# Performance work log

Measured on AMD Instinct MI355X. Metric: run time of the kernel, lower is better.

The kernel has to match this reference:

```python
import jax, jax.numpy as jnp
import numpy as np

T = 0.2
EPS = 1e-05


def setup_inputs() -> dict:
    key = jax.random.key(0)
    k1, k2 = jax.random.split(key)
    N, D, NUM_CLASSES = 8192, 128, 128
    inp = jax.random.normal(k1, (N, D), dtype=jnp.float32)
    label = jax.random.randint(k2, (N,), 0, NUM_CLASSES, dtype=jnp.int64)
    return {"input": inp, "label": label}


def reference(input, label):
    # Pairwise cosine similarity: dot(x_i, x_j) / max(||x_i|| * ||x_j||, eps)
    norms = jnp.sqrt(jnp.sum(input * input, axis=1))            # [N]
    denom = jnp.maximum(norms[:, None] * norms[None, :], EPS)   # [N, N]
    sim = (input @ input.T) / denom                             # [N, N]

    mask = (label[:, None] == label[None, :]).astype(input.dtype)  # same-label mask
    e = jnp.exp(sim / T)
    e = e - jnp.diag(jnp.diag(e))                               # zero the diagonal

    pos = mask * e                                              # positives (diag already 0)
    unsim = jnp.sum(e - pos, axis=-1, keepdims=True)            # [N, 1] negatives row-sum
    ratio = pos / (pos + unsim)                                 # per-pair NT-Xent prob
    safe = jnp.where(ratio > 0, ratio, 1.0)                     # loss[loss<=0] = 1
    loss_sum = jnp.sum(-jnp.log(safe))

    # number of off-diagonal positive pairs
    off_diag_mask = mask - jnp.diag(jnp.diag(mask))
    n_pos = jnp.count_nonzero(off_diag_mask).astype(input.dtype)
    return loss_sum / n_pos
```

## Files before the change

### kernel.cpp

```cpp
#include <hip/hip_runtime.h>
#include <math.h>

typedef float f32x4 __attribute__((ext_vector_type(4)));
typedef __attribute__((address_space(3))) unsigned int lds_u32;
typedef __attribute__((address_space(1))) const unsigned int glb_u32;

__global__ __launch_bounds__(256) void norm_kernel(
    const float* __restrict__ X, unsigned char* __restrict__ Y8,
    float* __restrict__ out, float inv_sqrtT) {
  int t = threadIdx.x;
  int row = blockIdx.x * 8 + (t >> 5);
  int l32 = t & 31;
  float4 v = ((const float4*)(X + (size_t)row * 128))[l32];
  float s = v.x * v.x + v.y * v.y + v.z * v.z + v.w * v.w;
  s += __shfl_xor(s, 1);
  s += __shfl_xor(s, 2);
  s += __shfl_xor(s, 4);
  s += __shfl_xor(s, 8);
  s += __shfl_xor(s, 16);
  float inv = inv_sqrtT * rsqrtf(fmaxf(s, 1e-24f));
  int pk = __builtin_amdgcn_cvt_pk_fp8_f32(v.x * inv, v.y * inv, 0, false);
  pk = __builtin_amdgcn_cvt_pk_fp8_f32(v.z * inv, v.w * inv, pk, true);
  int chunk = l32 >> 2;
  int off = ((chunk ^ (row & 7)) << 4) + ((l32 & 3) << 2);
  *(unsigned int*)(Y8 + (size_t)row * 128 + off) = (unsigned)pk;
  if (blockIdx.x == 0 && t == 0) out[0] = 0.f;
}

__global__ __launch_bounds__(256, 4) void pass1_kernel(
    const unsigned char* __restrict__ Y8, const int* __restrict__ lab,
    float* __restrict__ P, float* __restrict__ Q, float* __restrict__ S,
    int N) {
  __shared__ unsigned char As[128][128];
  __shared__ unsigned char Bs[2][64][128];
  __shared__ int labR[128];
  __shared__ float sS[4];

  const int b = blockIdx.x;
  const int bi = b >> 4, c = b & 15;
  const int i0 = bi * 128;
  const int j0 = c * 512;
  const int t = threadIdx.x;
  const int w = t >> 6, lane = t & 63;

#pragma unroll
  for (int k = 0; k < 4; ++k) {
    const int c0 = w * 64 + k * 256;
    const int cc = c0 + lane;
    __builtin_amdgcn_global_load_lds(
        (glb_u32*)(Y8 + (size_t)i0 * 128 + (size_t)cc * 16),
        (lds_u32*)((unsigned char*)&As[0][0] + c0 * 16), 16, 0, 0);
  }
#pragma unroll
  for (int k = 0; k < 2; ++k) {
    const int c0 = w * 64 + k * 256;
    const int cc = c0 + lane;
    __builtin_amdgcn_global_load_lds(
        (glb_u32*)(Y8 + (size_t)j0 * 128 + (size_t)cc * 16),
        (lds_u32*)((unsigned char*)&Bs[0][0][0] + c0 * 16), 16, 0, 0);
  }
  if (t < 128) labR[t] = lab[i0 + t];
  __syncthreads();

  const int quad = lane >> 4, l16 = lane & 15;
  const int rbase = w * 32;
  const int sw = l16 & 7;

  int lr[2][4];
#pragma unroll
  for (int pi = 0; pi < 2; ++pi)
#pragma unroll
    for (int r = 0; r < 4; ++r)
      lr[pi][r] = labR[rbase + pi * 16 + quad * 4 + r];

  float trow[2][4] = {};
  float pr[2][4] = {};
  float sacc = 0.f;

  for (int jt = 0; jt < 8; ++jt) {
    const int cur = jt & 1;
    const int jt0 = j0 + jt * 64;

    if (jt < 7) {
      const unsigned char* src = Y8 + (size_t)(jt0 + 64) * 128;
      unsigned char* dst = (unsigned char*)&Bs[cur ^ 1][0][0];
#pragma unroll
      for (int k = 0; k < 2; ++k) {
        const int c0 = w * 64 + k * 256;
        const int cc = c0 + lane;
        __builtin_amdgcn_global_load_lds((glb_u32*)(src + (size_t)cc * 16),
                                         (lds_u32*)(dst + c0 * 16), 16, 0, 0);
      }
    }

    int lc[4], cg[4];
#pragma unroll
    for (int pj = 0; pj < 4; ++pj) {
      cg[pj] = jt0 + pj * 16 + l16;
      lc[pj] = lab[cg[pj]];
    }

    f32x4 acc[2][4] = {};
#pragma unroll
    for (int ks = 0; ks < 4; ++ks) {
      const int ch = ks * 2 + (quad >> 1);
      const int off = ((ch ^ sw) << 4) + ((quad & 1) << 3);
      long af[2], bf[4];
#pragma unroll
      for (int p = 0; p < 2; ++p)
        af[p] = *(const long*)&As[rbase + p * 16 + l16][off];
#pragma unroll
      for (int p = 0; p < 4; ++p)
        bf[p] = *(const long*)&Bs[cur][p * 16 + l16][off];
#pragma unroll
      for (int pi = 0; pi < 2; ++pi)
#pragma unroll
        for (int pj = 0; pj < 4; ++pj)
          acc[pi][pj] = __builtin_amdgcn_mfma_f32_16x16x32_fp8_fp8(
              af[pi], bf[pj], acc[pi][pj], 0, 0, 0);
    }

    const bool dphase = ((jt0 >> 7) == bi);
    if (dphase) {
#pragma unroll
      for (int pi = 0; pi < 2; ++pi)
#pragma unroll
        for (int pj = 0; pj < 4; ++pj)
#pragma unroll
          for (int r = 0; r < 4; ++r) {
            const float s = acc[pi][pj][r];
            const float e = __expf(s);
            const int rowl = rbase + pi * 16 + quad * 4 + r;
            const bool self = (i0 + rowl) == cg[pj];
            const bool match = (lr[pi][r] == lc[pj]) && !self;
            trow[pi][r] += self ? 0.f : e;
            pr[pi][r] += match ? e : 0.f;
            sacc += match ? s : 0.f;
          }
    } else {
#pragma unroll
      for (int pi = 0; pi < 2; ++pi)
#pragma unroll
        for (int pj = 0; pj < 4; ++pj)
#pragma unroll
          for (int r = 0; r < 4; ++r) {
            const float s = acc[pi][pj][r];
            const float e = __expf(s);
            const bool match = (lr[pi][r] == lc[pj]);
            trow[pi][r] += e;
            pr[pi][r] += match ? e : 0.f;
            sacc += match ? s : 0.f;
          }
    }
    __syncthreads();
  }

#pragma unroll
  for (int pi = 0; pi < 2; ++pi)
#pragma unroll
    for (int r = 0; r < 4; ++r) {
      float v = trow[pi][r], q = pr[pi][r];
      v += __shfl_xor(v, 1);
      q += __shfl_xor(q, 1);
      v += __shfl_xor(v, 2);
      q += __shfl_xor(q, 2);
      v += __shfl_xor(v, 4);
      q += __shfl_xor(q, 4);
      v += __shfl_xor(v, 8);
      q += __shfl_xor(q, 8);
      if (l16 == 0) {
        const int row = rbase + pi * 16 + quad * 4 + r;
        P[c * N + i0 + row] = v;
        Q[c * N + i0 + row] = q;
      }
    }
#pragma unroll
  for (int m = 1; m < 64; m <<= 1) sacc += __shfl_xor(sacc, m);
  if (lane == 0) sS[w] = sacc;
  __syncthreads();
  if (t == 0) S[b] = sS[0] + sS[1] + sS[2] + sS[3];
}

__global__ __launch_bounds__(256) void finalize_kernel(
    const int* __restrict__ lab, const float* __restrict__ P,
    const float* __restrict__ Q, const float* __restrict__ S,
    float* __restrict__ out, int N) {
  __shared__ int hist[256];
  __shared__ float red[4];
  const int b = blockIdx.x, t = threadIdx.x;
  const int lane = t & 63, w = t >> 6;
  hist[t] = 0;
  __syncthreads();
  for (int i = t; i < N; i += 256) atomicAdd(&hist[lab[i] & 255], 1);
  __syncthreads();

  const int i = b * 256 + t;
  float tot = 0.f, p = 0.f;
#pragma unroll
  for (int cc = 0; cc < 16; ++cc) {
    tot += P[cc * N + i];
    p += Q[cc * N + i];
  }
  const float u = tot - p;
  const float cnti = (float)(hist[lab[i] & 255] - 1);
  float local = cnti * __logf(u) + p / u;
  if (t < 32) local -= S[b * 32 + t];
#pragma unroll
  for (int m = 1; m < 64; m <<= 1) local += __shfl_xor(local, m);
  if (lane == 0) red[w] = local;
  __syncthreads();
  if (t == 0) {
    float np = 0.f;
    for (int k = 0; k < 256; ++k) {
      const float m = (float)hist[k];
      np += m * m;
    }
    atomicAdd(out, (red[0] + red[1] + red[2] + red[3]) / (np - (float)N));
  }
}

extern "C" void kernel_launch(void* const* d_in, const int* in_sizes, int n_in,
                              void* d_out, int out_size, void* d_ws,
                              size_t ws_size, hipStream_t stream) {
  const float* X = (const float*)d_in[0];
  const int* lab = (const int*)d_in[1];
  float* out = (float*)d_out;

  const int N = in_sizes[1];

  unsigned char* Y8 = (unsigned char*)d_ws;
  float* P = (float*)(Y8 + (size_t)N * 128);
  float* Q = P + 16 * (size_t)N;
  float* S = Q + 16 * (size_t)N;

  const float inv_sqrtT = 2.2360679775f;
  norm_kernel<<<N / 8, 256, 0, stream>>>(X, Y8, out, inv_sqrtT);

  const int nblk = (N / 128) * 16;
  pass1_kernel<<<nblk, 256, 0, stream>>>(Y8, lab, P, Q, S, N);
  finalize_kernel<<<N / 256, 256, 0, stream>>>(lab, P, Q, S, out, N);
}
```

Before: 98.40 us.

## Drop LDS staging, load fp8 MFMA fragments from global, use exp2 scaling

Removes the LDS tiles and the async global-to-LDS double buffering. The A fragments are now kept in registers and the B fragments are read straight from global memory (the tile is small and should hit in cache), which also drops the per-tile barriers and the swizzled layout. The input scale now folds in log2(e), so the kernel can use exp2f in place of expf, and the diagonal-sum term is converted back by multiplying with ln2. The cost is more global and L2 traffic per MFMA with no LDS reuse across waves, and loads may be less coalesced.

New measurement: 138.7 us. 1.41x slower.

```diff
diff --git a/kernel.cpp b/kernel.cpp
--- a/kernel.cpp
+++ b/kernel.cpp
@@ -2,12 +2,11 @@
 #include <math.h>
 
 typedef float f32x4 __attribute__((ext_vector_type(4)));
-typedef __attribute__((address_space(3))) unsigned int lds_u32;
-typedef __attribute__((address_space(1))) const unsigned int glb_u32;
+
 
 __global__ __launch_bounds__(256) void norm_kernel(
     const float* __restrict__ X, unsigned char* __restrict__ Y8,
-    float* __restrict__ out, float inv_sqrtT) {
+    float* __restrict__ out, float scaleAB) {
   int t = threadIdx.x;
   int row = blockIdx.x * 8 + (t >> 5);
   int l32 = t & 31;
@@ -18,12 +17,10 @@
   s += __shfl_xor(s, 4);
   s += __shfl_xor(s, 8);
   s += __shfl_xor(s, 16);
-  float inv = inv_sqrtT * rsqrtf(fmaxf(s, 1e-24f));
+  float inv = scaleAB * rsqrtf(fmaxf(s, 1e-24f));
   int pk = __builtin_amdgcn_cvt_pk_fp8_f32(v.x * inv, v.y * inv, 0, false);
   pk = __builtin_amdgcn_cvt_pk_fp8_f32(v.z * inv, v.w * inv, pk, true);
-  int chunk = l32 >> 2;
-  int off = ((chunk ^ (row & 7)) << 4) + ((l32 & 3) << 2);
-  *(unsigned int*)(Y8 + (size_t)row * 128 + off) = (unsigned)pk;
+  *(unsigned int*)(Y8 + (size_t)row * 128 + l32 * 4) = (unsigned)pk;
   if (blockIdx.x == 0 && t == 0) out[0] = 0.f;
 }
 
@@ -31,9 +28,6 @@
     const unsigned char* __restrict__ Y8, const int* __restrict__ lab,
     float* __restrict__ P, float* __restrict__ Q, float* __restrict__ S,
     int N) {
-  __shared__ unsigned char As[128][128];
-  __shared__ unsigned char Bs[2][64][128];
-  __shared__ int labR[128];
   __shared__ float sS[4];
 
   const int b = blockIdx.x;
@@ -42,82 +36,53 @@
   const int j0 = c * 512;
   const int t = threadIdx.x;
   const int w = t >> 6, lane = t & 63;
-
-#pragma unroll
-  for (int k = 0; k < 4; ++k) {
-    const int c0 = w * 64 + k * 256;
-    const int cc = c0 + lane;
-    __builtin_amdgcn_global_load_lds(
-        (glb_u32*)(Y8 + (size_t)i0 * 128 + (size_t)cc * 16),
-        (lds_u32*)((unsigned char*)&As[0][0] + c0 * 16), 16, 0, 0);
-  }
-#pragma unroll
-  for (int k = 0; k < 2; ++k) {
-    const int c0 = w * 64 + k * 256;
-    const int cc = c0 + lane;
-    __builtin_amdgcn_global_load_lds(
-        (glb_u32*)(Y8 + (size_t)j0 * 128 + (size_t)cc * 16),
-        (lds_u32*)((unsigned char*)&Bs[0][0][0] + c0 * 16), 16, 0, 0);
-  }
-  if (t < 128) labR[t] = lab[i0 + t];
-  __syncthreads();
-
   const int quad = lane >> 4, l16 = lane & 15;
   const int rbase = w * 32;
-  const int sw = l16 & 7;
+  const int colb = quad * 8;
+
+  long af[4][2];
+#pragma unroll
+  for (int ks = 0; ks < 4; ++ks)
+#pragma unroll
+    for (int p = 0; p < 2; ++p)
+      af[ks][p] = *(const long*)(Y8 +
+                                 (size_t)(i0 + rbase + p * 16 + l16) * 128 +
+                                 ks * 32 + colb);
 
   int lr[2][4];
 #pragma unroll
   for (int pi = 0; pi < 2; ++pi)
 #pragma unroll
     for (int r = 0; r < 4; ++r)
-      lr[pi][r] = labR[rbase + pi * 16 + quad * 4 + r];
+      lr[pi][r] = lab[i0 + rbase + pi * 16 + quad * 4 + r];
 
   float trow[2][4] = {};
   float pr[2][4] = {};
   float sacc = 0.f;
 
+#pragma unroll 2
   for (int jt = 0; jt < 8; ++jt) {
-    const int cur = jt & 1;
     const int jt0 = j0 + jt * 64;
 
-    if (jt < 7) {
-      const unsigned char* src = Y8 + (size_t)(jt0 + 64) * 128;
-      unsigned char* dst = (unsigned char*)&Bs[cur ^ 1][0][0];
-#pragma unroll
-      for (int k = 0; k < 2; ++k) {
-        const int c0 = w * 64 + k * 256;
-        const int cc = c0 + lane;
-        __builtin_amdgcn_global_load_lds((glb_u32*)(src + (size_t)cc * 16),
-                                         (lds_u32*)(dst + c0 * 16), 16, 0, 0);
-      }
-    }
-
-    int lc[4], cg[4];
-#pragma unroll
-    for (int pj = 0; pj < 4; ++pj) {
-      cg[pj] = jt0 + pj * 16 + l16;
-      lc[pj] = lab[cg[pj]];
-    }
+    int lc[4];
+#pragma unroll
+    for (int pj = 0; pj < 4; ++pj) lc[pj] = lab[jt0 + pj * 16 + l16];
 
     f32x4 acc[2][4] = {};
 #pragma unroll
     for (int ks = 0; ks < 4; ++ks) {
-      const int ch = ks * 2 + (quad >> 1);
-      const int off = ((ch ^ sw) << 4) + ((quad & 1) << 3);
-      long af[2], bf[4];
-#pragma unroll
-      for (int p = 0; p < 2; ++p)
-        af[p] = *(const long*)&As[rbase + p * 16 + l16][off];
+      long bf[4];
 #pragma unroll
       for (int p = 0; p < 4; ++p)
-        bf[p] = *(const long*)&Bs[cur][p * 16 + l16][off];
+        bf[p] = *(const long*)(Y8 +
+                               (size_t)(jt0 + p * 16 + l16) * 128 +
+                               ks * 32 + colb);
 #pragma unroll
       for (int pi = 0; pi < 2; ++pi)
 #pragma unroll
         for (int pj = 0; pj < 4; ++pj)
           acc[pi][pj] = __builtin_amdgcn_mfma_f32_16x16x32_fp8_fp8(
-              af[pi], bf[pj], acc[pi][pj], 0, 0, 0);
+              af[ks][pi], bf[pj], acc[pi][pj], 0, 0, 0);
     }
 
     const bool dphase = ((jt0 >> 7) == bi);
@@ -128,14 +93,14 @@
         for (int pj = 0; pj < 4; ++pj)
 #pragma unroll
           for (int r = 0; r < 4; ++r) {
-            const float s = acc[pi][pj][r];
-            const float e = __expf(s);
+            const float s2 = acc[pi][pj][r];
+            const float e = exp2f(s2);
             const int rowl = rbase + pi * 16 + quad * 4 + r;
-            const bool self = (i0 + rowl) == cg[pj];
+            const bool self = (i0 + rowl) == (jt0 + pj * 16 + l16);
             const bool match = (lr[pi][r] == lc[pj]) && !self;
             trow[pi][r] += self ? 0.f : e;
             pr[pi][r] += match ? e : 0.f;
-            sacc += match ? s : 0.f;
+            sacc += match ? s2 : 0.f;
           }
     } else {
 #pragma unroll
@@ -144,15 +109,14 @@
         for (int pj = 0; pj < 4; ++pj)
 #pragma unroll
           for (int r = 0; r < 4; ++r) {
-            const float s = acc[pi][pj][r];
-            const float e = __expf(s);
+            const float s2 = acc[pi][pj][r];
+            const float e = exp2f(s2);
             const bool match = (lr[pi][r] == lc[pj]);
             trow[pi][r] += e;
             pr[pi][r] += match ? e : 0.f;
-            sacc += match ? s : 0.f;
+            sacc += match ? s2 : 0.f;
           }
     }
-    __syncthreads();
   }
 
 #pragma unroll
@@ -178,7 +142,8 @@
   for (int m = 1; m < 64; m <<= 1) sacc += __shfl_xor(sacc, m);
   if (lane == 0) sS[w] = sacc;
   __syncthreads();
-  if (t == 0) S[b] = sS[0] + sS[1] + sS[2] + sS[3];
+  if (t == 0)
+    S[b] = (sS[0] + sS[1] + sS[2] + sS[3]) * 0.69314718056f;
 }
 
 __global__ __launch_bounds__(256) void finalize_kernel(
@@ -233,10 +198,11 @@
   float* Q = P + 16 * (size_t)N;
   float* S = Q + 16 * (size_t)N;
 
-  const float inv_sqrtT = 2.2360679775f;
-  norm_kernel<<<N / 8, 256, 0, stream>>>(X, Y8, out, inv_sqrtT);
+  const float scaleAB = 2.68579102f;
+
+  norm_kernel<<<N / 8, 256, 0, stream>>>(X, Y8, out, scaleAB);
 
   const int nblk = (N / 128) * 16;
   pass1_kernel<<<nblk, 256, 0, stream>>>(Y8, lab, P, Q, S, N);
-  finalize_kernel<<<N / 256, 256, 0, stream>>>(lab, P, Q, S, out, N);
-}
+  finalize_kernel<<<32, 256, 0, stream>>>(lab, P, Q, S, out, N);
+}
```

## Shrink row tile to 64, keep A fragments in registers, fold exp scale into base 2

Applied to the files above, without the earlier changes.

Each block of the similarity pass now covers 64 rows instead of 128. A fragments are loaded straight from global memory into registers, so the As LDS tile and label staging are gone, and launch bounds allow 6 waves per SIMD. The normalisation scale now includes the factor log2(e), so the kernel can use exp2f. The positive-similarity sum is multiplied by ln2 to compensate. The grid doubles and B tiles are reloaded twice as often per row, trading less reuse for higher occupancy and cheaper exponentials.

Measured after the change: 100.4 us. About the same (+2.0%).

```diff
diff --git a/kernel.cpp b/kernel.cpp
--- a/kernel.cpp
+++ b/kernel.cpp
@@ -5,9 +5,10 @@
 typedef __attribute__((address_space(3))) unsigned int lds_u32;
 typedef __attribute__((address_space(1))) const unsigned int glb_u32;
 
+
 __global__ __launch_bounds__(256) void norm_kernel(
     const float* __restrict__ X, unsigned char* __restrict__ Y8,
-    float* __restrict__ out, float inv_sqrtT) {
+    float* __restrict__ out, float scaleAB) {
   int t = threadIdx.x;
   int row = blockIdx.x * 8 + (t >> 5);
   int l32 = t & 31;
@@ -18,7 +19,7 @@
   s += __shfl_xor(s, 4);
   s += __shfl_xor(s, 8);
   s += __shfl_xor(s, 16);
-  float inv = inv_sqrtT * rsqrtf(fmaxf(s, 1e-24f));
+  float inv = scaleAB * rsqrtf(fmaxf(s, 1e-24f));
   int pk = __builtin_amdgcn_cvt_pk_fp8_f32(v.x * inv, v.y * inv, 0, false);
   pk = __builtin_amdgcn_cvt_pk_fp8_f32(v.z * inv, v.w * inv, pk, true);
   int chunk = l32 >> 2;
@@ -27,30 +28,23 @@
   if (blockIdx.x == 0 && t == 0) out[0] = 0.f;
 }
 
-__global__ __launch_bounds__(256, 4) void pass1_kernel(
+__global__ __launch_bounds__(256, 6) void pass1_kernel(
     const unsigned char* __restrict__ Y8, const int* __restrict__ lab,
     float* __restrict__ P, float* __restrict__ Q, float* __restrict__ S,
     int N) {
-  __shared__ unsigned char As[128][128];
   __shared__ unsigned char Bs[2][64][128];
-  __shared__ int labR[128];
   __shared__ float sS[4];
 
   const int b = blockIdx.x;
   const int bi = b >> 4, c = b & 15;
-  const int i0 = bi * 128;
+  const int i0 = bi * 64;
   const int j0 = c * 512;
   const int t = threadIdx.x;
   const int w = t >> 6, lane = t & 63;
-
-#pragma unroll
-  for (int k = 0; k < 4; ++k) {
-    const int c0 = w * 64 + k * 256;
-    const int cc = c0 + lane;
-    __builtin_amdgcn_global_load_lds(
-        (glb_u32*)(Y8 + (size_t)i0 * 128 + (size_t)cc * 16),
-        (lds_u32*)((unsigned char*)&As[0][0] + c0 * 16), 16, 0, 0);
-  }
+  const int quad = lane >> 4, l16 = lane & 15;
+  const int rbase = w * 16;
+  const int sw = l16 & 7;
+
 #pragma unroll
   for (int k = 0; k < 2; ++k) {
     const int c0 = w * 64 + k * 256;
@@ -59,23 +53,26 @@
         (glb_u32*)(Y8 + (size_t)j0 * 128 + (size_t)cc * 16),
         (lds_u32*)((unsigned char*)&Bs[0][0][0] + c0 * 16), 16, 0, 0);
   }
-  if (t < 128) labR[t] = lab[i0 + t];
-  __syncthreads();
-
-  const int quad = lane >> 4, l16 = lane & 15;
-  const int rbase = w * 32;
-  const int sw = l16 & 7;
-
-  int lr[2][4];
-#pragma unroll
-  for (int pi = 0; pi < 2; ++pi)
-#pragma unroll
-    for (int r = 0; r < 4; ++r)
-      lr[pi][r] = labR[rbase + pi * 16 + quad * 4 + r];
-
-  float trow[2][4] = {};
-  float pr[2][4] = {};
+
+  long af[4];
+  {
+    const size_t abase = (size_t)(i0 + rbase + l16) * 128;
+#pragma unroll
+    for (int ks = 0; ks < 4; ++ks) {
+      const int ch = ks * 2 + (quad >> 1);
+      const int off = ((ch ^ sw) << 4) + ((quad & 1) << 3);
+      af[ks] = *(const long*)(Y8 + abase + off);
+    }
+  }
+  int lr[4];
+#pragma unroll
+  for (int r = 0; r < 4; ++r) lr[r] = lab[i0 + rbase + quad * 4 + r];
+
+  float trow[4] = {};
+  float pr[4] = {};
   float sacc = 0.f;
+
+  __syncthreads();
 
   for (int jt = 0; jt < 8; ++jt) {
     const int cur = jt & 1;
@@ -93,92 +90,78 @@
       }
     }
 
-    int lc[4], cg[4];
-#pragma unroll
-    for (int pj = 0; pj < 4; ++pj) {
-      cg[pj] = jt0 + pj * 16 + l16;
-      lc[pj] = lab[cg[pj]];
-    }
-
-    f32x4 acc[2][4] = {};
+    int lc[4];
+#pragma unroll
+    for (int pj = 0; pj < 4; ++pj) lc[pj] = lab[jt0 + pj * 16 + l16];
+
+    f32x4 acc[4] = {};
 #pragma unroll
     for (int ks = 0; ks < 4; ++ks) {
       const int ch = ks * 2 + (quad >> 1);
       const int off = ((ch ^ sw) << 4) + ((quad & 1) << 3);
-      long af[2], bf[4];
-#pragma unroll
-      for (int p = 0; p < 2; ++p)
-        af[p] = *(const long*)&As[rbase + p * 16 + l16][off];
+      long bf[4];
 #pragma unroll
       for (int p = 0; p < 4; ++p)
         bf[p] = *(const long*)&Bs[cur][p * 16 + l16][off];
 #pragma unroll
-      for (int pi = 0; pi < 2; ++pi)
-#pragma unroll
-        for (int pj = 0; pj < 4; ++pj)
-          acc[pi][pj] = __builtin_amdgcn_mfma_f32_16x16x32_fp8_fp8(
-              af[pi], bf[pj], acc[pi][pj], 0, 0, 0);
-    }
-
-    const bool dphase = ((jt0 >> 7) == bi);
-    if (dphase) {
-#pragma unroll
-      for (int pi = 0; pi < 2; ++pi)
-#pragma unroll
-        for (int pj = 0; pj < 4; ++pj)
-#pragma unroll
-          for (int r = 0; r < 4; ++r) {
-            const float s = acc[pi][pj][r];
-            const float e = __expf(s);
-            const int rowl = rbase + pi * 16 + quad * 4 + r;
-            const bool self = (i0 + rowl) == cg[pj];
-            const bool match = (lr[pi][r] == lc[pj]) && !self;
-            trow[pi][r] += self ? 0.f : e;
-            pr[pi][r] += match ? e : 0.f;
-            sacc += match ? s : 0.f;
-          }
+      for (int pj = 0; pj < 4; ++pj)
+        acc[pj] = __builtin_amdgcn_mfma_f32_16x16x32_fp8_fp8(af[ks], bf[pj],
+                                                             acc[pj], 0, 0, 0);
+    }
+
+    if (jt0 == i0) {
+#pragma unroll
+      for (int pj = 0; pj < 4; ++pj)
+#pragma unroll
+        for (int r = 0; r < 4; ++r) {
+          const float s2 = acc[pj][r];
+          const float e = exp2f(s2);
+          const int rowl = rbase + quad * 4 + r;
+          const bool self = rowl == (pj * 16 + l16);
+          const bool match = (lr[r] == lc[pj]) && !self;
+          trow[r] += self ? 0.f : e;
+          pr[r] += match ? e : 0.f;
+          sacc += match ? s2 : 0.f;
+        }
     } else {
 #pragma unroll
-      for (int pi = 0; pi < 2; ++pi)
-#pragma unroll
-        for (int pj = 0; pj < 4; ++pj)
-#pragma unroll
-          for (int r = 0; r < 4; ++r) {
-            const float s = acc[pi][pj][r];
-            const float e = __expf(s);
-            const bool match = (lr[pi][r] == lc[pj]);
-            trow[pi][r] += e;
-            pr[pi][r] += match ? e : 0.f;
-            sacc += match ? s : 0.f;
-          }
+      for (int pj = 0; pj < 4; ++pj)
+#pragma unroll
+        for (int r = 0; r < 4; ++r) {
+          const float s2 = acc[pj][r];
+          const float e = exp2f(s2);
+          const bool match = (lr[r] == lc[pj]);
+          trow[r] += e;
+          pr[r] += match ? e : 0.f;
+          sacc += match ? s2 : 0.f;
+        }
     }
     __syncthreads();
   }
 
 #pragma unroll
-  for (int pi = 0; pi < 2; ++pi)
-#pragma unroll
-    for (int r = 0; r < 4; ++r) {
-      float v = trow[pi][r], q = pr[pi][r];
-      v += __shfl_xor(v, 1);
-      q += __shfl_xor(q, 1);
-      v += __shfl_xor(v, 2);
-      q += __shfl_xor(q, 2);
-      v += __shfl_xor(v, 4);
-      q += __shfl_xor(q, 4);
-      v += __shfl_xor(v, 8);
-      q += __shfl_xor(q, 8);
-      if (l16 == 0) {
-        const int row = rbase + pi * 16 + quad * 4 + r;
-        P[c * N + i0 + row] = v;
-        Q[c * N + i0 + row] = q;
-      }
-    }
+  for (int r = 0; r < 4; ++r) {
+    float v = trow[r], q = pr[r];
+    v += __shfl_xor(v, 1);
+    q += __shfl_xor(q, 1);
+    v += __shfl_xor(v, 2);
+    q += __shfl_xor(q, 2);
+    v += __shfl_xor(v, 4);
+    q += __shfl_xor(q, 4);
+    v += __shfl_xor(v, 8);
+    q += __shfl_xor(q, 8);
+    if (l16 == 0) {
+      const int row = rbase + quad * 4 + r;
+      P[c * N + i0 + row] = v;
+      Q[c * N + i0 + row] = q;
+    }
+  }
 #pragma unroll
   for (int m = 1; m < 64; m <<= 1) sacc += __shfl_xor(sacc, m);
   if (lane == 0) sS[w] = sacc;
   __syncthreads();
-  if (t == 0) S[b] = sS[0] + sS[1] + sS[2] + sS[3];
+  if (t == 0)
+    S[b] = (sS[0] + sS[1] + sS[2] + sS[3]) * 0.69314718056f;
 }
 
 __global__ __launch_bounds__(256) void finalize_kernel(
@@ -204,7 +187,7 @@
   const float u = tot - p;
   const float cnti = (float)(hist[lab[i] & 255] - 1);
   float local = cnti * __logf(u) + p / u;
-  if (t < 32) local -= S[b * 32 + t];
+  if (t < 64) local -= S[b * 64 + t];
 #pragma unroll
   for (int m = 1; m < 64; m <<= 1) local += __shfl_xor(local, m);
   if (lane == 0) red[w] = local;
@@ -233,10 +216,11 @@
   float* Q = P + 16 * (size_t)N;
   float* S = Q + 16 * (size_t)N;
 
-  const float inv_sqrtT = 2.2360679775f;
-  norm_kernel<<<N / 8, 256, 0, stream>>>(X, Y8, out, inv_sqrtT);
-
-  const int nblk = (N / 128) * 16;
+  const float scaleAB = 2.68579102f;
+
+  norm_kernel<<<N / 8, 256, 0, stream>>>(X, Y8, out, scaleAB);
+
+  const int nblk = (N / 64) * 16;
   pass1_kernel<<<nblk, 256, 0, stream>>>(Y8, lab, P, Q, S, N);
-  finalize_kernel<<<N / 256, 256, 0, stream>>>(lab, P, Q, S, out, N);
-}
+  finalize_kernel<<<32, 256, 0, stream>>>(lab, P, Q, S, out, N);
+}
```
